# Kernel optimization log

Measured on AMD Instinct MI355X. Metric: run time of the kernel, lower is better.

The kernel has to match this reference:

```python
import jax, jax.numpy as jnp
import numpy as np

OFFSET_FP32 = np.uint32(1064828928)  # L-mul exponent-bias correction constant for float32


def lmul_matmul(A, B):
    """Approximate A @ B (m,n)x(n,p) via integer-add-as-multiply on float bit patterns.

    Torch ref adds bit patterns in int64 then truncates with .to(torch.uint32),
    i.e. arithmetic mod 2**32 -- identical to plain uint32 wraparound addition,
    so we stay in uint32 and avoid needing x64 mode.
    """
    Au = jax.lax.bitcast_convert_type(A, jnp.uint32)          # (m, n)
    Bu = jax.lax.bitcast_convert_type(B, jnp.uint32)          # (n, p)
    prod_bits = Au[:, :, None] + Bu[None, :, :] - OFFSET_FP32  # (m, n, p), wraps mod 2^32
    prod = jax.lax.bitcast_convert_type(prod_bits, jnp.float32)
    return prod.sum(axis=1)                                    # (m, p)


def setup_inputs() -> dict:
    key = jax.random.key(0)
    k1, k2, k3 = jax.random.split(key, 3)
    m, n, p = 256, 512, 512
    x = jax.random.normal(k1, (m, n), dtype=jnp.float32)
    bound = 1.0 / np.sqrt(n)  # kaiming_uniform(a=sqrt(5)) -> U(-1/sqrt(fan_in), 1/sqrt(fan_in))
    weight = jax.random.uniform(k2, (p, n), dtype=jnp.float32, minval=-bound, maxval=bound)
    bias = jax.random.uniform(k3, (p,), dtype=jnp.float32, minval=-bound, maxval=bound)
    return {"x": x, "weight": weight, "bias": bias}


def reference(x, weight, bias):
    out = lmul_matmul(x, weight.T)
    return out + bias
```

## Files before the change

kernel.cpp:

```cpp
#include <hip/hip_runtime.h>
#include <stdint.h>


#define OFFSET_FP32 1064828928u

constexpr int M = 256;
constexpr int N = 512;
constexpr int P = 512;

constexpr int BM = 8;
constexpr int BP = 64;
constexpr int TM = 4;
constexpr int NQ = 4;
constexpr int QK = 128;

__global__ __launch_bounds__(512) void lmul_linear_kernel(
    const uint32_t* __restrict__ xb,
    const uint32_t* __restrict__ wb,
    const float*    __restrict__ bias,
    float*          __restrict__ out)
{
    __shared__ uint32_t Bs[NQ][BP][QK];
    __shared__ float    Red[4][BM][BP];

    const int tid  = threadIdx.x;
    const int lane = tid & 63;
    const int wq   = __builtin_amdgcn_readfirstlane(tid >> 6);
    const int ks   = wq & 3;
    const int mq   = wq >> 2;

    const int p0 = blockIdx.y * BP;
    const int m0 = blockIdx.x * BM + mq * TM;

    const int g    = lane & 31;
    const int rsel = lane >> 5;

    auto qload = [&](int q, uint4* r) {
        #pragma unroll
        for (int i = 0; i < 4; ++i) {
            const int row = wq * 8 + i * 2 + rsel;
            r[i] = *(const uint4*)(wb + (size_t)(p0 + row) * N + q * QK + g * 4);
        }
    };
    auto qwrite1 = [&](int q, uint4 v, int i) {
        const int row = wq * 8 + i * 2 + rsel;
        v.x -= OFFSET_FP32; v.y -= OFFSET_FP32;
        v.z -= OFFSET_FP32; v.w -= OFFSET_FP32;
        *(uint4*)&Bs[q][row][(g ^ (row & 7)) * 4] = v;
    };

    float acc[TM][4] = {};
    const int rot = lane & 7;

    const uint32_t* xr0 = xb + (size_t)(m0 + 0) * N;
    const uint32_t* xr1 = xb + (size_t)(m0 + 1) * N;
    const uint32_t* xr2 = xb + (size_t)(m0 + 2) * N;
    const uint32_t* xr3 = xb + (size_t)(m0 + 3) * N;

    auto computeq = [&](int q, bool feed, int qn, uint4* r) {
        const uint32_t* brow = &Bs[q][lane][ks * 32];
        const int xoff = q * QK + ks * 32;
        #pragma unroll
        for (int j = 0; j < 8; ++j) {
            const uint4 b  = *(const uint4*)&brow[(j ^ rot) * 4];
            const uint4 a0 = *(const uint4*)(xr0 + xoff + j * 4);
            const uint4 a1 = *(const uint4*)(xr1 + xoff + j * 4);
            const uint4 a2 = *(const uint4*)(xr2 + xoff + j * 4);
            const uint4 a3 = *(const uint4*)(xr3 + xoff + j * 4);
            acc[0][0] += __uint_as_float(a0.x + b.x);
            acc[0][1] += __uint_as_float(a0.y + b.y);
            acc[0][2] += __uint_as_float(a0.z + b.z);
            acc[0][3] += __uint_as_float(a0.w + b.w);
            acc[1][0] += __uint_as_float(a1.x + b.x);
            acc[1][1] += __uint_as_float(a1.y + b.y);
            acc[1][2] += __uint_as_float(a1.z + b.z);
            acc[1][3] += __uint_as_float(a1.w + b.w);
            acc[2][0] += __uint_as_float(a2.x + b.x);
            acc[2][1] += __uint_as_float(a2.y + b.y);
            acc[2][2] += __uint_as_float(a2.z + b.z);
            acc[2][3] += __uint_as_float(a2.w + b.w);
            acc[3][0] += __uint_as_float(a3.x + b.x);
            acc[3][1] += __uint_as_float(a3.y + b.y);
            acc[3][2] += __uint_as_float(a3.z + b.z);
            acc[3][3] += __uint_as_float(a3.w + b.w);
            if (feed && (j & 1)) qwrite1(qn, r[j >> 1], j >> 1);
        }
    };

    auto lds_barrier = [&]() {
        asm volatile("s_waitcnt lgkmcnt(0)" ::: "memory");
        __builtin_amdgcn_s_barrier();
        __builtin_amdgcn_sched_barrier(0);
    };

    uint4 ra[4], rb[4];
    qload(0, ra);
    #pragma unroll
    for (int i = 0; i < 4; ++i) qwrite1(0, ra[i], i);
    qload(1, rb);
    lds_barrier();

    qload(2, ra);
    computeq(0, true, 1, rb);
    lds_barrier();

    qload(3, rb);
    computeq(1, true, 2, ra);
    lds_barrier();

    computeq(2, true, 3, rb);
    lds_barrier();

    computeq(3, false, 0, nullptr);

    #pragma unroll
    for (int r = 0; r < TM; ++r)
        Red[ks][mq * TM + r][lane] =
            (acc[r][0] + acc[r][1]) + (acc[r][2] + acc[r][3]);
    __syncthreads();

    const int rr = tid >> 6;
    const int p  = p0 + lane;
    const float s = (Red[0][rr][lane] + Red[1][rr][lane])
                  + (Red[2][rr][lane] + Red[3][rr][lane]);
    out[(size_t)(blockIdx.x * BM + rr) * P + p] = s + bias[p];
}

extern "C" void kernel_launch(void* const* d_in, const int* in_sizes, int n_in,
                              void* d_out, int out_size, void* d_ws, size_t ws_size,
                              hipStream_t stream) {
    const uint32_t* xb   = (const uint32_t*)d_in[0];
    const uint32_t* wb   = (const uint32_t*)d_in[1];
    const float*    bias = (const float*)d_in[2];
    float*          out  = (float*)d_out;

    dim3 grid(M / BM, P / BP);
    dim3 block(512);
    lmul_linear_kernel<<<grid, block, 0, stream>>>(xb, wb, bias, out);
}
```

Measured before the change: 63.64 us.

## Split first K-quarter into half-stages to shorten prologue and trim reduction traffic

```diff
diff --git a/kernel.cpp b/kernel.cpp
--- a/kernel.cpp
+++ b/kernel.cpp
@@ -49,6 +49,24 @@
         *(uint4*)&Bs[q][row][(g ^ (row & 7)) * 4] = v;
     };
 
+    const int ge    = lane & 15;
+    const int ersel = lane >> 4;
+
+    auto eload = [&](int e, uint4* r) {
+        #pragma unroll
+        for (int i = 0; i < 2; ++i) {
+            const int row = wq * 8 + i * 4 + ersel;
+            r[i] = *(const uint4*)(wb + (size_t)(p0 + row) * N + e * 64 + ge * 4);
+        }
+    };
+    auto ewrite1 = [&](int e, uint4 v, int i) {
+        const int row = wq * 8 + i * 4 + ersel;
+        const int G   = e * 16 + ge;
+        v.x -= OFFSET_FP32; v.y -= OFFSET_FP32;
+        v.z -= OFFSET_FP32; v.w -= OFFSET_FP32;
+        *(uint4*)&Bs[0][row][(G ^ (row & 7)) * 4] = v;
+    };
+
     float acc[TM][4] = {};
     const int rot = lane & 7;
 
@@ -57,32 +75,45 @@
     const uint32_t* xr2 = xb + (size_t)(m0 + 2) * N;
     const uint32_t* xr3 = xb + (size_t)(m0 + 3) * N;
 
-    auto computeq = [&](int q, bool feed, int qn, uint4* r) {
-        const uint32_t* brow = &Bs[q][lane][ks * 32];
-        const int xoff = q * QK + ks * 32;
+    auto step = [&](const uint32_t* bq, int slot, int xoff) {
+        const uint4 b  = *(const uint4*)&bq[slot * 4];
+        const uint4 a0 = *(const uint4*)(xr0 + xoff);
+        const uint4 a1 = *(const uint4*)(xr1 + xoff);
+        const uint4 a2 = *(const uint4*)(xr2 + xoff);
+        const uint4 a3 = *(const uint4*)(xr3 + xoff);
+        acc[0][0] += __uint_as_float(a0.x + b.x);
+        acc[0][1] += __uint_as_float(a0.y + b.y);
+        acc[0][2] += __uint_as_float(a0.z + b.z);
+        acc[0][3] += __uint_as_float(a0.w + b.w);
+        acc[1][0] += __uint_as_float(a1.x + b.x);
+        acc[1][1] += __uint_as_float(a1.y + b.y);
+        acc[1][2] += __uint_as_float(a1.z + b.z);
+        acc[1][3] += __uint_as_float(a1.w + b.w);
+        acc[2][0] += __uint_as_float(a2.x + b.x);
+        acc[2][1] += __uint_as_float(a2.y + b.y);
+        acc[2][2] += __uint_as_float(a2.z + b.z);
+        acc[2][3] += __uint_as_float(a2.w + b.w);
+        acc[3][0] += __uint_as_float(a3.x + b.x);
+        acc[3][1] += __uint_as_float(a3.y + b.y);
+        acc[3][2] += __uint_as_float(a3.z + b.z);
+        acc[3][3] += __uint_as_float(a3.w + b.w);
+    };
+
+    auto compute_e = [&](int e, int feedmode, uint4* r) {
+        const uint32_t* bq = &Bs[0][lane][0];
+        #pragma unroll
+        for (int j = 0; j < 4; ++j) {
+            step(bq, (e * 16 + ks * 4 + j) ^ rot, e * 64 + ks * 16 + j * 4);
+            if (feedmode == 1 && j >= 2) ewrite1(1, r[j - 2], j - 2);
+            if (feedmode == 2) qwrite1(1, r[j], j);
+        }
+    };
+
+    auto compute_q = [&](int q, bool feed, int qn, uint4* r) {
+        const uint32_t* bq = &Bs[q][lane][0];
         #pragma unroll
         for (int j = 0; j < 8; ++j) {
-            const uint4 b  = *(const uint4*)&brow[(j ^ rot) * 4];
-            const uint4 a0 = *(const uint4*)(xr0 + xoff + j * 4);
-            const uint4 a1 = *(const uint4*)(xr1 + xoff + j * 4);
-            const uint4 a2 = *(const uint4*)(xr2 + xoff + j * 4);
-            const uint4 a3 = *(const uint4*)(xr3 + xoff + j * 4);
-            acc[0][0] += __uint_as_float(a0.x + b.x);
-            acc[0][1] += __uint_as_float(a0.y + b.y);
-            acc[0][2] += __uint_as_float(a0.z + b.z);
-            acc[0][3] += __uint_as_float(a0.w + b.w);
-            acc[1][0] += __uint_as_float(a1.x + b.x);
-            acc[1][1] += __uint_as_float(a1.y + b.y);
-            acc[1][2] += __uint_as_float(a1.z + b.z);
-            acc[1][3] += __uint_as_float(a1.w + b.w);
-            acc[2][0] += __uint_as_float(a2.x + b.x);
-            acc[2][1] += __uint_as_float(a2.y + b.y);
-            acc[2][2] += __uint_as_float(a2.z + b.z);
-            acc[2][3] += __uint_as_float(a2.w + b.w);
-            acc[3][0] += __uint_as_float(a3.x + b.x);
-            acc[3][1] += __uint_as_float(a3.y + b.y);
-            acc[3][2] += __uint_as_float(a3.z + b.z);
-            acc[3][3] += __uint_as_float(a3.w + b.w);
+            step(bq, ks * 8 + (j ^ rot), q * QK + ks * 32 + j * 4);
             if (feed && (j & 1)) qwrite1(qn, r[j >> 1], j >> 1);
         }
     };
@@ -93,37 +124,46 @@
         __builtin_amdgcn_sched_barrier(0);
     };
 
-    uint4 ra[4], rb[4];
-    qload(0, ra);
-    #pragma unroll
-    for (int i = 0; i < 4; ++i) qwrite1(0, ra[i], i);
-    qload(1, rb);
+    uint4 ea[2], eb[2], ra[4], rb[4];
+    eload(0, ea);
+    ewrite1(0, ea[0], 0);
+    ewrite1(0, ea[1], 1);
+    eload(1, eb);
+    qload(1, ra);
     lds_barrier();
 
-    qload(2, ra);
-    computeq(0, true, 1, rb);
+    qload(2, rb);
+    compute_e(0, 1, eb);
     lds_barrier();
 
-    qload(3, rb);
-    computeq(1, true, 2, ra);
+    compute_e(1, 2, ra);
     lds_barrier();
 
-    computeq(2, true, 3, rb);
+    qload(3, ra);
+    compute_q(1, true, 2, rb);
     lds_barrier();
 
-    computeq(3, false, 0, nullptr);
+    compute_q(2, true, 3, ra);
+    lds_barrier();
+
+    compute_q(3, false, 0, nullptr);
 
     #pragma unroll
-    for (int r = 0; r < TM; ++r)
-        Red[ks][mq * TM + r][lane] =
-            (acc[r][0] + acc[r][1]) + (acc[r][2] + acc[r][3]);
-    __syncthreads();
+    for (int r = 0; r < TM; ++r) {
+        if (r != ks)
+            Red[ks][mq * TM + r][lane] =
+                (acc[r][0] + acc[r][1]) + (acc[r][2] + acc[r][3]);
+    }
+    lds_barrier();
 
-    const int rr = tid >> 6;
-    const int p  = p0 + lane;
-    const float s = (Red[0][rr][lane] + Red[1][rr][lane])
-                  + (Red[2][rr][lane] + Red[3][rr][lane]);
-    out[(size_t)(blockIdx.x * BM + rr) * P + p] = s + bias[p];
+    const int Rrow = mq * TM + ks;
+    float s = (acc[ks][0] + acc[ks][1]) + (acc[ks][2] + acc[ks][3]);
+    #pragma unroll
+    for (int k2 = 0; k2 < 4; ++k2)
+        if (k2 != ks) s += Red[k2][Rrow][lane];
+
+    const int p = p0 + lane;
+    out[(size_t)(blockIdx.x * BM + Rrow) * P + p] = s + bias[p];
 }
 
 extern "C" void kernel_launch(void* const* d_in, const int* in_sizes, int n_in,
```

Result: slower. 69.03 us (+8.5%).
